# Kernel optimization log

Measured on AMD Instinct MI355X. Metric: run time of the kernel, lower is better.

## Reference

```python
import jax, jax.numpy as jnp
from jax import lax
import numpy as np

H = 64  # LSTM_HIDDEN_DIM
I = 3   # NUM_WEATHER_FEATURES


def _lstm_layer(x_seq, w_ih, w_hh, b_ih, b_hh):
    # x_seq: [B, T, in]; w_ih: [4H, in]; w_hh: [4H, H]; b_*: [4H]
    B = x_seq.shape[0]
    # Precompute input projections for all timesteps: [T, B, 4H]
    gx = jnp.einsum('bti,gi->tbg', x_seq, w_ih) + (b_ih + b_hh)
    h0 = jnp.zeros((B, H), dtype=x_seq.dtype)
    c0 = jnp.zeros((B, H), dtype=x_seq.dtype)

    def step(carry, g_t):
        h, c = carry
        gates = g_t + h @ w_hh.T  # [B, 4H]
        i, f, g, o = jnp.split(gates, 4, axis=-1)  # PyTorch gate order i,f,g,o
        i = jax.nn.sigmoid(i)
        f = jax.nn.sigmoid(f)
        g = jnp.tanh(g)
        o = jax.nn.sigmoid(o)
        c = f * c + i * g
        h = o * jnp.tanh(c)
        return (h, c), h

    (h_T, _), hs = lax.scan(step, (h0, c0), gx)
    # hs: [T, B, H] -> [B, T, H]
    return jnp.transpose(hs, (1, 0, 2)), h_T


def setup_inputs() -> dict:
    key = jax.random.key(0)
    ks = jax.random.split(key, 9)
    s = 1.0 / np.sqrt(H)  # PyTorch LSTM init scale
    x = jax.random.normal(ks[0], (4096, 365, I), dtype=jnp.float32)
    return {
        'x': x,
        'w_ih0': jax.random.uniform(ks[1], (4 * H, I), jnp.float32, -s, s),
        'w_hh0': jax.random.uniform(ks[2], (4 * H, H), jnp.float32, -s, s),
        'b_ih0': jax.random.uniform(ks[3], (4 * H,), jnp.float32, -s, s),
        'b_hh0': jax.random.uniform(ks[4], (4 * H,), jnp.float32, -s, s),
        'w_ih1': jax.random.uniform(ks[5], (4 * H, H), jnp.float32, -s, s),
        'w_hh1': jax.random.uniform(ks[6], (4 * H, H), jnp.float32, -s, s),
        'b_ih1': jax.random.uniform(ks[7], (4 * H,), jnp.float32, -s, s),
        'b_hh1': jax.random.uniform(ks[8], (4 * H,), jnp.float32, -s, s),
    }


def reference(x, w_ih0, w_hh0, b_ih0, b_hh0, w_ih1, w_hh1, b_ih1, b_hh1):
    # Layer 1 over raw features
    h1_seq, _ = _lstm_layer(x, w_ih0, w_hh0, b_ih0, b_hh0)
    # Layer 2 over layer-1 hidden states (eval mode: inter-layer dropout disabled)
    _, h2_T = _lstm_layer(h1_seq, w_ih1, w_hh1, b_ih1, b_hh1)
    # forward returns h_n[-1] == final hidden state of top layer: [B, H]
    return h2_T
```

## Files before the change

kernel.cpp:

```cpp
#include <hip/hip_runtime.h>

#define TT 365
#define NB 16
#define NTH 1024
#define XLEN (NB * TT * 3)

typedef _Float16 halfx8 __attribute__((ext_vector_type(8)));
typedef float floatx4 __attribute__((ext_vector_type(4)));

#define MMH(A, B, C) __builtin_amdgcn_mfma_f32_16x16x32_f16((A), (B), (C), 0, 0, 0)

__device__ __forceinline__ float sigm2(float y) {
  return __builtin_amdgcn_rcpf(1.0f + __builtin_amdgcn_exp2f(y));
}
__device__ __forceinline__ float tanh2(float y) {
  return fmaf(2.0f, __builtin_amdgcn_rcpf(1.0f + __builtin_amdgcn_exp2f(y)), -1.0f);
}
__device__ __forceinline__ float tanhc(float c) {
  float e = __builtin_amdgcn_exp2f(-2.8853900817779268f * c);
  return fmaf(2.0f, __builtin_amdgcn_rcpf(1.0f + e), -1.0f);
}
__device__ __forceinline__ unsigned short h16(float v) {
  _Float16 h = (_Float16)v;
  return __builtin_bit_cast(unsigned short, h);
}

#define LOADFRAG(SRC, SCALE, HI)                                               \
  do {                                                                         \
    _Pragma("unroll")                                                          \
    for (int jj = 0; jj < 8; ++jj) {                                           \
      (HI)[jj] = (_Float16)((SCALE) * (SRC)[jj]);                              \
    }                                                                          \
  } while (0)

#define E_PHASE(ZW)                                                            \
  do {                                                                         \
    floatx4 e = b1v;                                                           \
    e = MMH(a2h[0], bh0, e); e = MMH(a2h[1], bh1, e);                          \
    e = MMH(a2h[2], bh2, e); e = MMH(a2h[3], bh3, e);                          \
    const float i2 = sigm2(e[0]), f2s = sigm2(e[1]);                           \
    const float gg = tanh2(e[2]), o2 = sigm2(e[3]);                            \
    c2 = fmaf(f2s, c2, i2 * gg);                                               \
    const float h2v = o2 * tanhc(c2);                                          \
    (ZW)[sidx2] = h16(h2v);                                                    \
  } while (0)

#define D_PHASE(ZW)                                                            \
  do {                                                                         \
    const floatx4 s0 = {xv0, xv0, xv0, xv0};                                   \
    const floatx4 s1 = {xv1, xv1, xv1, xv1};                                   \
    const floatx4 s2 = {xv2, xv2, xv2, xv2};                                   \
    floatx4 d = __builtin_elementwise_fma(wiX, s0,                             \
                  __builtin_elementwise_fma(wiY, s1,                           \
                    __builtin_elementwise_fma(wiZ, s2, b0v)));                 \
    d = MMH(a1h[0], bh0, d); d = MMH(a1h[1], bh1, d);                          \
    const float i1 = sigm2(d[0]), f1s = sigm2(d[1]);                           \
    const float gg = tanh2(d[2]), o1 = sigm2(d[3]);                            \
    c1 = fmaf(f1s, c1, i1 * gg);                                               \
    const float h1v = o1 * tanhc(c1);                                          \
    (ZW)[sidx1] = h16(h1v);                                                    \
  } while (0)

#define STEP(ZR, ZW)                                                           \
  do {                                                                         \
    const halfx8* __restrict__ Z8 = (const halfx8*)(ZR);                       \
    const halfx8 bh0 = Z8[lane],       bh1 = Z8[64 + lane];                    \
    const halfx8 bh2 = Z8[128 + lane], bh3 = Z8[192 + lane];                   \
    const float xv0 = xp[0], xv1 = xp[1], xv2 = xp[2];                         \
    if (grpA) { E_PHASE(ZW); D_PHASE(ZW); }                                    \
    else      { D_PHASE(ZW); E_PHASE(ZW); }                                    \
    xp += 3;                                                                   \
    __syncthreads();                                                           \
  } while (0)

__global__ __launch_bounds__(NTH)
__attribute__((amdgpu_waves_per_eu(4, 4)))
void lstm2_mfma7(
    const float* __restrict__ x,
    const float* __restrict__ w_ih0, const float* __restrict__ w_hh0,
    const float* __restrict__ b_ih0, const float* __restrict__ b_hh0,
    const float* __restrict__ w_ih1, const float* __restrict__ w_hh1,
    const float* __restrict__ b_ih1, const float* __restrict__ b_hh1,
    float* __restrict__ out)
{
  __shared__ __align__(16) unsigned short Z[2][2048];
  __shared__ __align__(16) float xlds[XLEN];

  const int tid  = threadIdx.x;
  const int lane = tid & 63;
  const int wv   = tid >> 6;
  const int n15  = lane & 15;
  const int quad = lane >> 4;
  const int bbase = blockIdx.x * NB;
  const bool grpA = ((wv >> 2) & 1) == 0;

  const float SS = -1.4426950408889634f;
  const float SG = -2.8853900817779268f;
  const float sA = ((n15 & 3) == 2) ? SG : SS;

  halfx8 a1h[2];
  halfx8 a2h[4];
  floatx4 wiX, wiY, wiZ, b0v, b1v;

  {
    const int mt   = wv;
    const int arow = (n15 & 3) * 64 + mt * 4 + (n15 >> 2);
    #pragma unroll
    for (int kt = 0; kt < 2; ++kt) {
      const float* src = w_hh0 + arow * 64 + kt * 32 + quad * 8;
      LOADFRAG(src, sA, a1h[kt]);
    }
    #pragma unroll
    for (int kt = 0; kt < 4; ++kt) {
      const int k0 = kt * 32 + quad * 8;
      const float* src = (k0 < 64) ? (w_ih1 + arow * 64 + k0)
                                   : (w_hh1 + arow * 64 + (k0 - 64));
      LOADFRAG(src, sA, a2h[kt]);
    }
    #pragma unroll
    for (int r = 0; r < 4; ++r) {
      const int crow = r * 64 + mt * 4 + quad;
      const float sC = (r == 2) ? SG : SS;
      wiX[r] = sC * w_ih0[crow * 3 + 0];
      wiY[r] = sC * w_ih0[crow * 3 + 1];
      wiZ[r] = sC * w_ih0[crow * 3 + 2];
      b0v[r] = sC * (b_ih0[crow] + b_hh0[crow]);
      b1v[r] = sC * (b_ih1[crow] + b_hh1[crow]);
    }
  }

  const int j = wv * 4 + quad;
  const int sidx1 = (j >> 5) * 512 + ((j >> 3) & 3) * 128 + n15 * 8 + (j & 7);
  const int sidx2 = sidx1 + 1024;

  {
    const float* xg = x + (size_t)bbase * (TT * 3);
    for (int i = tid; i < XLEN; i += NTH) xlds[i] = xg[i];
    for (int i = tid; i < 2048; i += NTH) { Z[0][i] = 0; Z[1][i] = 0; }
  }

  float c1 = 0.f, c2 = 0.f;
  unsigned short* const Zb0 = &Z[0][0];
  unsigned short* const Zb1 = &Z[1][0];

  __syncthreads();

  {
    const float xv0 = xlds[n15 * 1095 + 0];
    const float xv1 = xlds[n15 * 1095 + 1];
    const float xv2 = xlds[n15 * 1095 + 2];
    const float p0 = fmaf(wiX[0], xv0, fmaf(wiY[0], xv1, fmaf(wiZ[0], xv2, b0v[0])));
    const float p2 = fmaf(wiX[2], xv0, fmaf(wiY[2], xv1, fmaf(wiZ[2], xv2, b0v[2])));
    const float p3 = fmaf(wiX[3], xv0, fmaf(wiY[3], xv1, fmaf(wiZ[3], xv2, b0v[3])));
    const float ig = sigm2(p0), gg = tanh2(p2), og = sigm2(p3);
    c1 = ig * gg;
    Zb0[sidx1] = h16(og * tanhc(c1));
  }
  __syncthreads();

  const float* xp = xlds + n15 * 1095 + 3;
  for (int it = 0; it < 182; ++it) {
    STEP(Zb0, Zb1);
    STEP(Zb1, Zb0);
  }

  {
    const halfx8* __restrict__ Z8 = (const halfx8*)Zb0;
    const halfx8 bh0 = Z8[lane],       bh1 = Z8[64 + lane];
    const halfx8 bh2 = Z8[128 + lane], bh3 = Z8[192 + lane];
    floatx4 e = b1v;
    e = MMH(a2h[0], bh0, e); e = MMH(a2h[1], bh1, e);
    e = MMH(a2h[2], bh2, e); e = MMH(a2h[3], bh3, e);
    const float i2 = sigm2(e[0]), f2s = sigm2(e[1]);
    const float gg = tanh2(e[2]), o2 = sigm2(e[3]);
    c2 = fmaf(f2s, c2, i2 * gg);
    const float h2v = o2 * tanhc(c2);
    out[(size_t)(bbase + n15) * 64 + j] = h2v;
  }
}

extern "C" void kernel_launch(void* const* d_in, const int* in_sizes, int n_in,
                              void* d_out, int out_size, void* d_ws, size_t ws_size,
                              hipStream_t stream) {
  const float* x     = (const float*)d_in[0];
  const float* w_ih0 = (const float*)d_in[1];
  const float* w_hh0 = (const float*)d_in[2];
  const float* b_ih0 = (const float*)d_in[3];
  const float* b_hh0 = (const float*)d_in[4];
  const float* w_ih1 = (const float*)d_in[5];
  const float* w_hh1 = (const float*)d_in[6];
  const float* b_ih1 = (const float*)d_in[7];
  const float* b_hh1 = (const float*)d_in[8];
  float* out = (float*)d_out;

  const int B = in_sizes[0] / (TT * 3);
  const int grid = B / NB;

  lstm2_mfma7<<<dim3(grid), dim3(NTH), 0, stream>>>(
      x, w_ih0, w_hh0, b_ih0, b_hh0, w_ih1, w_hh1, b_ih1, b_hh1, out);
}
```

Before: 351.7 us.

## Specialize waves per LSTM layer and fuse gate nonlinearities with shared reciprocals

Result: faster. 311.9 us (-11.3%).

```diff
diff --git a/kernel.cpp b/kernel.cpp
--- a/kernel.cpp
+++ b/kernel.cpp
@@ -7,20 +7,17 @@
 
 typedef _Float16 halfx8 __attribute__((ext_vector_type(8)));
 typedef float floatx4 __attribute__((ext_vector_type(4)));
+typedef float floatx2 __attribute__((ext_vector_type(2)));
 
 #define MMH(A, B, C) __builtin_amdgcn_mfma_f32_16x16x32_f16((A), (B), (C), 0, 0, 0)
 
-__device__ __forceinline__ float sigm2(float y) {
-  return __builtin_amdgcn_rcpf(1.0f + __builtin_amdgcn_exp2f(y));
-}
-__device__ __forceinline__ float tanh2(float y) {
-  return fmaf(2.0f, __builtin_amdgcn_rcpf(1.0f + __builtin_amdgcn_exp2f(y)), -1.0f);
-}
-__device__ __forceinline__ float tanhc(float c) {
-  float e = __builtin_amdgcn_exp2f(-2.8853900817779268f * c);
-  return fmaf(2.0f, __builtin_amdgcn_rcpf(1.0f + e), -1.0f);
-}
-__device__ __forceinline__ unsigned short h16(float v) {
+#define SGP -2.8853900817779268f
+#define SGN  2.8853900817779268f
+#define SS_  -1.4426950408889634f
+
+static __device__ __forceinline__ float rcpf(float x) { return __builtin_amdgcn_rcpf(x); }
+static __device__ __forceinline__ float ex2(float x)  { return __builtin_amdgcn_exp2f(x); }
+static __device__ __forceinline__ unsigned short h16(float v) {
   _Float16 h = (_Float16)v;
   return __builtin_bit_cast(unsigned short, h);
 }
@@ -33,49 +30,36 @@
     }                                                                          \
   } while (0)
 
-#define E_PHASE(ZW)                                                            \
+#define PTAIL_CORE(PA, PB, CS2, HOUT)                                          \
+  const floatx2 one_ = {1.0f, 1.0f};                                           \
+  const floatx2 ei_ = {ex2((PA)[0]), ex2((PB)[0])};                            \
+  const floatx2 ef_ = {ex2((PA)[1]), ex2((PB)[1])};                            \
+  const floatx2 eg_ = {ex2((PA)[2]), ex2((PB)[2])};                            \
+  const floatx2 eo_ = {ex2((PA)[3]), ex2((PB)[3])};                            \
+  const floatx2 fd_ = one_ + ef_;                                              \
+  const floatx2 fr_ = {rcpf(fd_.x), rcpf(fd_.y)};                              \
+  const floatx2 P1_ = (one_ + ei_) * (one_ + eg_);                             \
+  const floatx2 R1_ = {rcpf(P1_.x), rcpf(P1_.y)};                              \
+  const floatx2 sgn2_ = {SGN, SGN};                                            \
+  const floatx2 sgp2_ = {SGP, SGP};                                            \
+  (CS2) = fr_ * (CS2) + (sgn2_ * eg_ + sgp2_) * R1_;                           \
+  (CS2).x = fminf((CS2).x, 126.0f);                                            \
+  (CS2).y = fminf((CS2).y, 126.0f);                                            \
+  const floatx2 ec_ = {ex2((CS2).x), ex2((CS2).y)};                            \
+  const floatx2 P2_ = (one_ + eo_) * (one_ + ec_);                             \
+  const floatx2 R2_ = {rcpf(P2_.x), rcpf(P2_.y)};                              \
+  const floatx2 HOUT = (one_ - ec_) * R2_;
+
+#define PTAIL(PA, PB, CS2, ZW, IA, IB)                                         \
   do {                                                                         \
-    floatx4 e = b1v;                                                           \
-    e = MMH(a2h[0], bh0, e); e = MMH(a2h[1], bh1, e);                          \
-    e = MMH(a2h[2], bh2, e); e = MMH(a2h[3], bh3, e);                          \
-    const float i2 = sigm2(e[0]), f2s = sigm2(e[1]);                           \
-    const float gg = tanh2(e[2]), o2 = sigm2(e[3]);                            \
-    c2 = fmaf(f2s, c2, i2 * gg);                                               \
-    const float h2v = o2 * tanhc(c2);                                          \
-    (ZW)[sidx2] = h16(h2v);                                                    \
-  } while (0)
-
-#define D_PHASE(ZW)                                                            \
-  do {                                                                         \
-    const floatx4 s0 = {xv0, xv0, xv0, xv0};                                   \
-    const floatx4 s1 = {xv1, xv1, xv1, xv1};                                   \
-    const floatx4 s2 = {xv2, xv2, xv2, xv2};                                   \
-    floatx4 d = __builtin_elementwise_fma(wiX, s0,                             \
-                  __builtin_elementwise_fma(wiY, s1,                           \
-                    __builtin_elementwise_fma(wiZ, s2, b0v)));                 \
-    d = MMH(a1h[0], bh0, d); d = MMH(a1h[1], bh1, d);                          \
-    const float i1 = sigm2(d[0]), f1s = sigm2(d[1]);                           \
-    const float gg = tanh2(d[2]), o1 = sigm2(d[3]);                            \
-    c1 = fmaf(f1s, c1, i1 * gg);                                               \
-    const float h1v = o1 * tanhc(c1);                                          \
-    (ZW)[sidx1] = h16(h1v);                                                    \
-  } while (0)
-
-#define STEP(ZR, ZW)                                                           \
-  do {                                                                         \
-    const halfx8* __restrict__ Z8 = (const halfx8*)(ZR);                       \
-    const halfx8 bh0 = Z8[lane],       bh1 = Z8[64 + lane];                    \
-    const halfx8 bh2 = Z8[128 + lane], bh3 = Z8[192 + lane];                   \
-    const float xv0 = xp[0], xv1 = xp[1], xv2 = xp[2];                         \
-    if (grpA) { E_PHASE(ZW); D_PHASE(ZW); }                                    \
-    else      { D_PHASE(ZW); E_PHASE(ZW); }                                    \
-    xp += 3;                                                                   \
-    __syncthreads();                                                           \
+    PTAIL_CORE(PA, PB, CS2, hv_)                                               \
+    (ZW)[IA] = h16(hv_.x);                                                     \
+    (ZW)[IB] = h16(hv_.y);                                                     \
   } while (0)
 
 __global__ __launch_bounds__(NTH)
 __attribute__((amdgpu_waves_per_eu(4, 4)))
-void lstm2_mfma7(
+void lstm2_mfma10(
     const float* __restrict__ x,
     const float* __restrict__ w_ih0, const float* __restrict__ w_hh0,
     const float* __restrict__ b_ih0, const float* __restrict__ b_hh0,
@@ -92,90 +76,151 @@
   const int n15  = lane & 15;
   const int quad = lane >> 4;
   const int bbase = blockIdx.x * NB;
-  const bool grpA = ((wv >> 2) & 1) == 0;
-
-  const float SS = -1.4426950408889634f;
-  const float SG = -2.8853900817779268f;
-  const float sA = ((n15 & 3) == 2) ? SG : SS;
-
-  halfx8 a1h[2];
-  halfx8 a2h[4];
-  floatx4 wiX, wiY, wiZ, b0v, b1v;
-
-  {
-    const int mt   = wv;
-    const int arow = (n15 & 3) * 64 + mt * 4 + (n15 >> 2);
-    #pragma unroll
-    for (int kt = 0; kt < 2; ++kt) {
-      const float* src = w_hh0 + arow * 64 + kt * 32 + quad * 8;
-      LOADFRAG(src, sA, a1h[kt]);
-    }
-    #pragma unroll
-    for (int kt = 0; kt < 4; ++kt) {
-      const int k0 = kt * 32 + quad * 8;
-      const float* src = (k0 < 64) ? (w_ih1 + arow * 64 + k0)
-                                   : (w_hh1 + arow * 64 + (k0 - 64));
-      LOADFRAG(src, sA, a2h[kt]);
-    }
-    #pragma unroll
-    for (int r = 0; r < 4; ++r) {
-      const int crow = r * 64 + mt * 4 + quad;
-      const float sC = (r == 2) ? SG : SS;
-      wiX[r] = sC * w_ih0[crow * 3 + 0];
-      wiY[r] = sC * w_ih0[crow * 3 + 1];
-      wiZ[r] = sC * w_ih0[crow * 3 + 2];
-      b0v[r] = sC * (b_ih0[crow] + b_hh0[crow]);
-      b1v[r] = sC * (b_ih1[crow] + b_hh1[crow]);
-    }
-  }
-
-  const int j = wv * 4 + quad;
-  const int sidx1 = (j >> 5) * 512 + ((j >> 3) & 3) * 128 + n15 * 8 + (j & 7);
-  const int sidx2 = sidx1 + 1024;
+  const float sA = ((n15 & 3) == 2) ? SGP : SS_;
 
   {
     const float* xg = x + (size_t)bbase * (TT * 3);
     for (int i = tid; i < XLEN; i += NTH) xlds[i] = xg[i];
     for (int i = tid; i < 2048; i += NTH) { Z[0][i] = 0; Z[1][i] = 0; }
   }
-
-  float c1 = 0.f, c2 = 0.f;
   unsigned short* const Zb0 = &Z[0][0];
   unsigned short* const Zb1 = &Z[1][0];
-
   __syncthreads();
 
-  {
-    const float xv0 = xlds[n15 * 1095 + 0];
-    const float xv1 = xlds[n15 * 1095 + 1];
-    const float xv2 = xlds[n15 * 1095 + 2];
-    const float p0 = fmaf(wiX[0], xv0, fmaf(wiY[0], xv1, fmaf(wiZ[0], xv2, b0v[0])));
-    const float p2 = fmaf(wiX[2], xv0, fmaf(wiY[2], xv1, fmaf(wiZ[2], xv2, b0v[2])));
-    const float p3 = fmaf(wiX[3], xv0, fmaf(wiY[3], xv1, fmaf(wiZ[3], xv2, b0v[3])));
-    const float ig = sigm2(p0), gg = tanh2(p2), og = sigm2(p3);
-    c1 = ig * gg;
-    Zb0[sidx1] = h16(og * tanhc(c1));
-  }
-  __syncthreads();
-
-  const float* xp = xlds + n15 * 1095 + 3;
-  for (int it = 0; it < 182; ++it) {
-    STEP(Zb0, Zb1);
-    STEP(Zb1, Zb0);
-  }
-
-  {
-    const halfx8* __restrict__ Z8 = (const halfx8*)Zb0;
-    const halfx8 bh0 = Z8[lane],       bh1 = Z8[64 + lane];
-    const halfx8 bh2 = Z8[128 + lane], bh3 = Z8[192 + lane];
-    floatx4 e = b1v;
-    e = MMH(a2h[0], bh0, e); e = MMH(a2h[1], bh1, e);
-    e = MMH(a2h[2], bh2, e); e = MMH(a2h[3], bh3, e);
-    const float i2 = sigm2(e[0]), f2s = sigm2(e[1]);
-    const float gg = tanh2(e[2]), o2 = sigm2(e[3]);
-    c2 = fmaf(f2s, c2, i2 * gg);
-    const float h2v = o2 * tanhc(c2);
-    out[(size_t)(bbase + n15) * 64 + j] = h2v;
+  if (wv < 8) {
+    const int w = wv;
+    halfx8 a2[2][4];
+    floatx4 b1v[2];
+    #pragma unroll
+    for (int tt = 0; tt < 2; ++tt) {
+      const int mt   = 2 * w + tt;
+      const int arow = (n15 & 3) * 64 + mt * 4 + (n15 >> 2);
+      #pragma unroll
+      for (int kt = 0; kt < 4; ++kt) {
+        const int k0 = kt * 32 + quad * 8;
+        const float* src = (k0 < 64) ? (w_ih1 + arow * 64 + k0)
+                                     : (w_hh1 + arow * 64 + (k0 - 64));
+        LOADFRAG(src, sA, a2[tt][kt]);
+      }
+      #pragma unroll
+      for (int r = 0; r < 4; ++r) {
+        const int crow = r * 64 + mt * 4 + quad;
+        const float sC = (r == 2) ? SGP : SS_;
+        b1v[tt][r] = sC * (b_ih1[crow] + b_hh1[crow]);
+      }
+    }
+    const int j0 = 8 * w + quad, j1 = 8 * w + 4 + quad;
+    const int si0 = 1024 + (j0 >> 5) * 512 + ((j0 >> 3) & 3) * 128 + n15 * 8 + (j0 & 7);
+    const int si1 = 1024 + (j1 >> 5) * 512 + ((j1 >> 3) & 3) * 128 + n15 * 8 + (j1 & 7);
+    floatx2 c2v = {0.f, 0.f};
+    const halfx8* const Z0r = (const halfx8*)Zb0 + lane;
+    const halfx8* const Z1r = (const halfx8*)Zb1 + lane;
+
+    __syncthreads();
+
+#define ESTEP(ZRP, ZW)                                                         \
+    do {                                                                       \
+      const halfx8 bh0 = (ZRP)[0],   bh1 = (ZRP)[64];                          \
+      const halfx8 bh2 = (ZRP)[128], bh3 = (ZRP)[192];                         \
+      floatx4 e0 = b1v[0], e1 = b1v[1];                                        \
+      e0 = MMH(a2[0][0], bh0, e0); e0 = MMH(a2[0][1], bh1, e0);                \
+      e0 = MMH(a2[0][2], bh2, e0); e0 = MMH(a2[0][3], bh3, e0);                \
+      e1 = MMH(a2[1][0], bh0, e1); e1 = MMH(a2[1][1], bh1, e1);                \
+      e1 = MMH(a2[1][2], bh2, e1); e1 = MMH(a2[1][3], bh3, e1);                \
+      PTAIL(e0, e1, c2v, ZW, si0, si1);                                        \
+      __syncthreads();                                                         \
+    } while (0)
+
+    for (int it = 0; it < 182; ++it) {
+      ESTEP(Z0r, Zb1);
+      ESTEP(Z1r, Zb0);
+    }
+
+    {
+      const halfx8 bh0 = Z0r[0],   bh1 = Z0r[64];
+      const halfx8 bh2 = Z0r[128], bh3 = Z0r[192];
+      floatx4 e0 = b1v[0], e1 = b1v[1];
+      e0 = MMH(a2[0][0], bh0, e0); e0 = MMH(a2[0][1], bh1, e0);
+      e0 = MMH(a2[0][2], bh2, e0); e0 = MMH(a2[0][3], bh3, e0);
+      e1 = MMH(a2[1][0], bh0, e1); e1 = MMH(a2[1][1], bh1, e1);
+      e1 = MMH(a2[1][2], bh2, e1); e1 = MMH(a2[1][3], bh3, e1);
+      PTAIL_CORE(e0, e1, c2v, hv_)
+      out[(size_t)(bbase + n15) * 64 + j0] = hv_.x;
+      out[(size_t)(bbase + n15) * 64 + j1] = hv_.y;
+    }
+  } else {
+    const int u = wv - 8;
+    halfx8 a1[2][2];
+    floatx4 wiX[2], wiY[2], wiZ[2], b0v[2];
+    #pragma unroll
+    for (int tt = 0; tt < 2; ++tt) {
+      const int mt   = 2 * u + tt;
+      const int arow = (n15 & 3) * 64 + mt * 4 + (n15 >> 2);
+      #pragma unroll
+      for (int kt = 0; kt < 2; ++kt) {
+        const float* src = w_hh0 + arow * 64 + kt * 32 + quad * 8;
+        LOADFRAG(src, sA, a1[tt][kt]);
+      }
+      #pragma unroll
+      for (int r = 0; r < 4; ++r) {
+        const int crow = r * 64 + mt * 4 + quad;
+        const float sC = (r == 2) ? SGP : SS_;
+        wiX[tt][r] = sC * w_ih0[crow * 3 + 0];
+        wiY[tt][r] = sC * w_ih0[crow * 3 + 1];
+        wiZ[tt][r] = sC * w_ih0[crow * 3 + 2];
+        b0v[tt][r] = sC * (b_ih0[crow] + b_hh0[crow]);
+      }
+    }
+    const int j0 = 8 * u + quad, j1 = 8 * u + 4 + quad;
+    const int si0 = (j0 >> 5) * 512 + ((j0 >> 3) & 3) * 128 + n15 * 8 + (j0 & 7);
+    const int si1 = (j1 >> 5) * 512 + ((j1 >> 3) & 3) * 128 + n15 * 8 + (j1 & 7);
+    floatx2 c1v = {0.f, 0.f};
+    const halfx8* const Z0r = (const halfx8*)Zb0 + lane;
+    const halfx8* const Z1r = (const halfx8*)Zb1 + lane;
+
+    {
+      const float xv0 = xlds[n15 * 1095 + 0];
+      const float xv1 = xlds[n15 * 1095 + 1];
+      const float xv2 = xlds[n15 * 1095 + 2];
+      const floatx4 s0 = {xv0, xv0, xv0, xv0};
+      const floatx4 s1 = {xv1, xv1, xv1, xv1};
+      const floatx4 s2 = {xv2, xv2, xv2, xv2};
+      floatx4 d0 = __builtin_elementwise_fma(wiX[0], s0,
+                     __builtin_elementwise_fma(wiY[0], s1,
+                       __builtin_elementwise_fma(wiZ[0], s2, b0v[0])));
+      floatx4 d1 = __builtin_elementwise_fma(wiX[1], s0,
+                     __builtin_elementwise_fma(wiY[1], s1,
+                       __builtin_elementwise_fma(wiZ[1], s2, b0v[1])));
+      PTAIL(d0, d1, c1v, Zb0, si0, si1);
+    }
+    __syncthreads();
+
+    const float* xp = xlds + n15 * 1095 + 3;
+
+#define DSTEP(ZRP, ZW)                                                         \
+    do {                                                                       \
+      const halfx8 bh0 = (ZRP)[0], bh1 = (ZRP)[64];                            \
+      const float xv0 = xp[0], xv1 = xp[1], xv2 = xp[2];                       \
+      const floatx4 s0 = {xv0, xv0, xv0, xv0};                                 \
+      const floatx4 s1 = {xv1, xv1, xv1, xv1};                                 \
+      const floatx4 s2 = {xv2, xv2, xv2, xv2};                                 \
+      floatx4 d0 = __builtin_elementwise_fma(wiX[0], s0,                       \
+                     __builtin_elementwise_fma(wiY[0], s1,                     \
+                       __builtin_elementwise_fma(wiZ[0], s2, b0v[0])));        \
+      floatx4 d1 = __builtin_elementwise_fma(wiX[1], s0,                       \
+                     __builtin_elementwise_fma(wiY[1], s1,                     \
+                       __builtin_elementwise_fma(wiZ[1], s2, b0v[1])));        \
+      d0 = MMH(a1[0][0], bh0, d0); d0 = MMH(a1[0][1], bh1, d0);                \
+      d1 = MMH(a1[1][0], bh0, d1); d1 = MMH(a1[1][1], bh1, d1);                \
+      PTAIL(d0, d1, c1v, ZW, si0, si1);                                        \
+      xp += 3;                                                                 \
+      __syncthreads();                                                         \
+    } while (0)
+
+    for (int it = 0; it < 182; ++it) {
+      DSTEP(Z0r, Zb1);
+      DSTEP(Z1r, Zb0);
+    }
   }
 }
 
@@ -196,6 +241,6 @@
   const int B = in_sizes[0] / (TT * 3);
   const int grid = B / NB;
 
-  lstm2_mfma7<<<dim3(grid), dim3(NTH), 0, stream>>>(
+  lstm2_mfma10<<<dim3(grid), dim3(NTH), 0, stream>>>(
       x, w_ih0, w_hh0, b_ih0, b_hh0, w_ih1, w_hh1, b_ih1, b_hh1, out);
 }
```
